# Performance work log

Measured on AMD Instinct MI355X. Metric: run time of the kernel, lower is better.

## Reference

```python
import jax, jax.numpy as jnp
import numpy as np

B, S, H, O, K = 32, 2048, 768, 768, 64


def setup_inputs() -> dict:
    key = jax.random.key(0)
    k0, k1, k2, k3, k4 = jax.random.split(key, 5)
    hidden = jax.random.normal(k0, (B, S, H), dtype=jnp.float32)
    token_idxs = jnp.sort(jax.random.randint(k1, (B, K), 0, S), axis=1)
    subject_hidden = jax.random.normal(k2, (B, H), dtype=jnp.float32)
    Wa = jax.random.normal(k3, (2 * H, 1), dtype=jnp.float32) * 0.02
    ba = jnp.zeros((1,), dtype=jnp.float32)
    Wo = jax.random.normal(k4, (H, O), dtype=jnp.float32) * 0.02
    bo = jnp.zeros((O,), dtype=jnp.float32)
    return {"hidden": hidden, "token_idxs": token_idxs, "subject_hidden": subject_hidden,
            "Wa": Wa, "ba": ba, "Wo": Wo, "bo": bo}


def reference(hidden, token_idxs, subject_hidden, Wa, ba, Wo, bo):
    b, s, h = hidden.shape
    # binary token mask [B,S] from per-example index lists (duplicates collapse to 1)
    mask = jnp.zeros((b, s), hidden.dtype).at[jnp.arange(b)[:, None], token_idxs].set(1.0)
    m3 = mask[:, :, None]                                  # [B,S,1]
    masked = hidden * m3                                   # masked_hidden
    subj_rep = subject_hidden[:, None, :] * m3             # broadcast + mask, no repeat
    # alignment_model(concat(subj, masked)) done as split matmul to avoid [B,S,2H]
    scores = subj_rep @ Wa[:h] + masked @ Wa[h:] + ba      # [B,S,1]
    # masked softmax over the selected tokens only (dim=0 over selected entries == seq axis)
    logits = jnp.where(m3 > 0, scores, jnp.float32(-1e9))
    attention_weights = jax.nn.softmax(logits, axis=1) * m3  # exact zeros off-mask
    pooled = jnp.einsum("bsh,bs->bh", masked, attention_weights[:, :, 0])
    transformed = jnp.tanh(pooled @ Wo + bo)
    return transformed, attention_weights
```

## Files before the change

kernel.cpp:

```cpp
#include <hip/hip_runtime.h>
#include <cmath>

#define Bb 32
#define Ss 2048
#define Hh 768
#define Oo 768
#define Kk 64

__global__ __launch_bounds__(256) void attn_pool_kernel(
    const float* __restrict__ hidden,
    const int*   __restrict__ idxs,
    const float* __restrict__ subj,
    const float* __restrict__ Wa,
    const float* __restrict__ ba,
    float* __restrict__ aw_out,
    float* __restrict__ pooled)
{
    const int b    = blockIdx.x;
    const int tid  = threadIdx.x;
    const int lane = tid & 63;
    const int wave = tid >> 6;

    __shared__ int   s_idx[Kk];
    __shared__ float s_aw[Kk];
    __shared__ float s_red[4];
    __shared__ float s_const;

    float4* awz = (float4*)(aw_out + (size_t)b * Ss);
    for (int i = tid; i < Ss / 4; i += 256) awz[i] = make_float4(0.f, 0.f, 0.f, 0.f);

    if (tid < Kk) s_idx[tid] = idxs[b * Kk + tid];
    __syncthreads();

    {
        float p = 0.f;
        for (int h = tid; h < Hh; h += 256)
            p += subj[b * Hh + h] * Wa[h];
        #pragma unroll
        for (int m = 32; m >= 1; m >>= 1) p += __shfl_xor(p, m);
        if (lane == 0) s_red[wave] = p;
        __syncthreads();
        if (tid == 0) s_const = s_red[0] + s_red[1] + s_red[2] + s_red[3] + ba[0];
        __syncthreads();
    }

    for (int j = wave; j < Kk; j += 4) {
        const float* row = hidden + ((size_t)b * Ss + s_idx[j]) * Hh;
        float p = 0.f;
        #pragma unroll
        for (int t = 0; t < Hh / 64; ++t)
            p += row[lane + 64 * t] * Wa[Hh + lane + 64 * t];
        #pragma unroll
        for (int m = 32; m >= 1; m >>= 1) p += __shfl_xor(p, m);
        if (lane == 0) s_aw[j] = p + s_const;
    }
    __syncthreads();

    if (wave == 0) {
        const int j = lane;
        const bool active = (j == 0) || (s_idx[j] != s_idx[j - 1]);
        float sc = active ? s_aw[j] : -3.0e38f;
        float mx = sc;
        #pragma unroll
        for (int m = 32; m >= 1; m >>= 1) mx = fmaxf(mx, __shfl_xor(mx, m));
        float e = active ? expf(sc - mx) : 0.f;
        float sum = e;
        #pragma unroll
        for (int m = 32; m >= 1; m >>= 1) sum += __shfl_xor(sum, m);
        const float aw = e / sum;
        s_aw[j] = aw;
        if (active) aw_out[(size_t)b * Ss + s_idx[j]] = aw;
    }
    __syncthreads();

    for (int h = tid; h < Hh; h += 256) {
        float acc = 0.f;
        #pragma unroll 8
        for (int j = 0; j < Kk; ++j)
            acc += s_aw[j] * hidden[((size_t)b * Ss + s_idx[j]) * Hh + h];
        pooled[b * Hh + h] = acc;
    }
}

__global__ __launch_bounds__(64) void gemm_tanh_kernel(
    const float* __restrict__ pooled,
    const float* __restrict__ Wo,
    const float* __restrict__ bo,
    float* __restrict__ out)
{
    const int b     = blockIdx.x / (Oo / 64);
    const int chunk = blockIdx.x % (Oo / 64);
    const int o     = chunk * 64 + threadIdx.x;

    __shared__ float p[Hh];
    float4* p4 = (float4*)p;
    const float4* src = (const float4*)(pooled + b * Hh);
    for (int i = threadIdx.x; i < Hh / 4; i += 64) p4[i] = src[i];
    __syncthreads();

    float a0 = 0.f, a1 = 0.f, a2 = 0.f, a3 = 0.f;
    #pragma unroll 4
    for (int h = 0; h < Hh; h += 4) {
        const float4 pv = *(const float4*)&p[h];
        a0 = fmaf(pv.x, Wo[(h + 0) * Oo + o], a0);
        a1 = fmaf(pv.y, Wo[(h + 1) * Oo + o], a1);
        a2 = fmaf(pv.z, Wo[(h + 2) * Oo + o], a2);
        a3 = fmaf(pv.w, Wo[(h + 3) * Oo + o], a3);
    }
    out[b * Oo + o] = tanhf(a0 + a1 + a2 + a3 + bo[o]);
}

extern "C" void kernel_launch(void* const* d_in, const int* in_sizes, int n_in,
                              void* d_out, int out_size, void* d_ws, size_t ws_size,
                              hipStream_t stream) {
    const float* hidden = (const float*)d_in[0];
    const int*   idxs   = (const int*)d_in[1];
    const float* subj   = (const float*)d_in[2];
    const float* Wa     = (const float*)d_in[3];
    const float* ba     = (const float*)d_in[4];
    const float* Wo     = (const float*)d_in[5];
    const float* bo     = (const float*)d_in[6];

    float* out    = (float*)d_out;
    float* aw_out = out + Bb * Oo;
    float* pooled = (float*)d_ws;

    attn_pool_kernel<<<Bb, 256, 0, stream>>>(hidden, idxs, subj, Wa, ba, aw_out, pooled);
    gemm_tanh_kernel<<<Bb * (Oo / 64), 64, 0, stream>>>(pooled, Wo, bo, out);
}
```

Measured before the change: 286.2 us.

## Split attention pooling into scores, softmax and fused pool-GEMM kernels for parallelism

The single 32-block attention kernel is replaced by a 512-block score kernel, with one wave per selected token and float4 loads, plus a small softmax kernel. A pooling+output GEMM kernel follows, where each of 96 blocks recomputes the pooled vector for its batch row and covers a 256-wide output slice. The aim is to spread the gather and score work across many more CUs than the 32 batch blocks could use. In exchange it adds a kernel launch, and the pooled gather is repeated three times per batch.

```diff
diff --git a/kernel.cpp b/kernel.cpp
--- a/kernel.cpp
+++ b/kernel.cpp
@@ -7,107 +7,131 @@
 #define Oo 768
 #define Kk 64
 
-__global__ __launch_bounds__(256) void attn_pool_kernel(
+__global__ __launch_bounds__(256) void scores_kernel(
     const float* __restrict__ hidden,
+    const int*   __restrict__ idxs,
+    const float* __restrict__ Wa,
+    float* __restrict__ scores,
+    float* __restrict__ aw_out)
+{
+    const int tid  = threadIdx.x;
+    const int lane = tid & 63;
+    const int wid  = blockIdx.x * 4 + (tid >> 6);
+    const int gid  = blockIdx.x * 256 + tid;
+
+    if (gid < (Bb * Ss / 4))
+        ((float4*)aw_out)[gid] = make_float4(0.f, 0.f, 0.f, 0.f);
+
+    const int b = wid >> 6;
+    const int j = wid & 63;
+    const int t_idx = idxs[b * Kk + j];
+
+    const float4* row4 = (const float4*)(hidden + ((size_t)b * Ss + t_idx) * Hh);
+    const float4* wa4  = (const float4*)(Wa + Hh);
+    float p = 0.f;
+    #pragma unroll
+    for (int t = 0; t < 3; ++t) {
+        const float4 r = row4[lane + 64 * t];
+        const float4 w = wa4[lane + 64 * t];
+        p += r.x * w.x + r.y * w.y + r.z * w.z + r.w * w.w;
+    }
+    #pragma unroll
+    for (int m = 32; m >= 1; m >>= 1) p += __shfl_xor(p, m);
+    if (lane == 0) scores[wid] = p;
+}
+
+__global__ __launch_bounds__(64) void softmax_kernel(
     const int*   __restrict__ idxs,
     const float* __restrict__ subj,
     const float* __restrict__ Wa,
     const float* __restrict__ ba,
-    float* __restrict__ aw_out,
-    float* __restrict__ pooled)
+    const float* __restrict__ scores,
+    float* __restrict__ aw,
+    float* __restrict__ aw_out)
 {
-    const int b    = blockIdx.x;
-    const int tid  = threadIdx.x;
-    const int lane = tid & 63;
-    const int wave = tid >> 6;
+    const int b = blockIdx.x;
+    const int j = threadIdx.x;
 
-    __shared__ int   s_idx[Kk];
-    __shared__ float s_aw[Kk];
-    __shared__ float s_red[4];
-    __shared__ float s_const;
+    const float4* s4  = (const float4*)(subj + b * Hh);
+    const float4* wa4 = (const float4*)Wa;
+    float p = 0.f;
+    #pragma unroll
+    for (int t = 0; t < 3; ++t) {
+        const float4 r = s4[j + 64 * t];
+        const float4 w = wa4[j + 64 * t];
+        p += r.x * w.x + r.y * w.y + r.z * w.z + r.w * w.w;
+    }
+    #pragma unroll
+    for (int m = 32; m >= 1; m >>= 1) p += __shfl_xor(p, m);
+    const float sconst = p + ba[0];
 
-    float4* awz = (float4*)(aw_out + (size_t)b * Ss);
-    for (int i = tid; i < Ss / 4; i += 256) awz[i] = make_float4(0.f, 0.f, 0.f, 0.f);
+    const int  myidx   = idxs[b * Kk + j];
+    const int  previdx = (j > 0) ? idxs[b * Kk + j - 1] : -1;
+    const bool active  = (j == 0) || (myidx != previdx);
 
-    if (tid < Kk) s_idx[tid] = idxs[b * Kk + tid];
-    __syncthreads();
+    float sc = active ? (scores[b * Kk + j] + sconst) : -3.0e38f;
+    float mx = sc;
+    #pragma unroll
+    for (int m = 32; m >= 1; m >>= 1) mx = fmaxf(mx, __shfl_xor(mx, m));
+    const float e = active ? expf(sc - mx) : 0.f;
+    float sum = e;
+    #pragma unroll
+    for (int m = 32; m >= 1; m >>= 1) sum += __shfl_xor(sum, m);
+    const float w = e / sum;
 
-    {
-        float p = 0.f;
-        for (int h = tid; h < Hh; h += 256)
-            p += subj[b * Hh + h] * Wa[h];
-        #pragma unroll
-        for (int m = 32; m >= 1; m >>= 1) p += __shfl_xor(p, m);
-        if (lane == 0) s_red[wave] = p;
-        __syncthreads();
-        if (tid == 0) s_const = s_red[0] + s_red[1] + s_red[2] + s_red[3] + ba[0];
-        __syncthreads();
-    }
-
-    for (int j = wave; j < Kk; j += 4) {
-        const float* row = hidden + ((size_t)b * Ss + s_idx[j]) * Hh;
-        float p = 0.f;
-        #pragma unroll
-        for (int t = 0; t < Hh / 64; ++t)
-            p += row[lane + 64 * t] * Wa[Hh + lane + 64 * t];
-        #pragma unroll
-        for (int m = 32; m >= 1; m >>= 1) p += __shfl_xor(p, m);
-        if (lane == 0) s_aw[j] = p + s_const;
-    }
-    __syncthreads();
-
-    if (wave == 0) {
-        const int j = lane;
-        const bool active = (j == 0) || (s_idx[j] != s_idx[j - 1]);
-        float sc = active ? s_aw[j] : -3.0e38f;
-        float mx = sc;
-        #pragma unroll
-        for (int m = 32; m >= 1; m >>= 1) mx = fmaxf(mx, __shfl_xor(mx, m));
-        float e = active ? expf(sc - mx) : 0.f;
-        float sum = e;
-        #pragma unroll
-        for (int m = 32; m >= 1; m >>= 1) sum += __shfl_xor(sum, m);
-        const float aw = e / sum;
-        s_aw[j] = aw;
-        if (active) aw_out[(size_t)b * Ss + s_idx[j]] = aw;
-    }
-    __syncthreads();
-
-    for (int h = tid; h < Hh; h += 256) {
-        float acc = 0.f;
-        #pragma unroll 8
-        for (int j = 0; j < Kk; ++j)
-            acc += s_aw[j] * hidden[((size_t)b * Ss + s_idx[j]) * Hh + h];
-        pooled[b * Hh + h] = acc;
-    }
+    aw[b * Kk + j] = w;
+    if (active) aw_out[(size_t)b * Ss + myidx] = w;
 }
 
-__global__ __launch_bounds__(64) void gemm_tanh_kernel(
-    const float* __restrict__ pooled,
+__global__ __launch_bounds__(1024) void pool_gemm_kernel(
+    const float* __restrict__ hidden,
+    const int*   __restrict__ idxs,
+    const float* __restrict__ aw,
     const float* __restrict__ Wo,
     const float* __restrict__ bo,
     float* __restrict__ out)
 {
-    const int b     = blockIdx.x / (Oo / 64);
-    const int chunk = blockIdx.x % (Oo / 64);
-    const int o     = chunk * 64 + threadIdx.x;
+    const int b   = blockIdx.x / 3;
+    const int oc  = blockIdx.x % 3;
+    const int tid = threadIdx.x;
 
-    __shared__ float p[Hh];
-    float4* p4 = (float4*)p;
-    const float4* src = (const float4*)(pooled + b * Hh);
-    for (int i = threadIdx.x; i < Hh / 4; i += 64) p4[i] = src[i];
+    __shared__ float s_aw[Kk];
+    __shared__ int   s_idx[Kk];
+    __shared__ float s_pool[Hh];
+    __shared__ float s_part[4 * 256];
+
+    if (tid < Kk) {
+        s_aw[tid]  = aw[b * Kk + tid];
+        s_idx[tid] = idxs[b * Kk + tid];
+    }
     __syncthreads();
 
-    float a0 = 0.f, a1 = 0.f, a2 = 0.f, a3 = 0.f;
-    #pragma unroll 4
-    for (int h = 0; h < Hh; h += 4) {
-        const float4 pv = *(const float4*)&p[h];
-        a0 = fmaf(pv.x, Wo[(h + 0) * Oo + o], a0);
-        a1 = fmaf(pv.y, Wo[(h + 1) * Oo + o], a1);
-        a2 = fmaf(pv.z, Wo[(h + 2) * Oo + o], a2);
-        a3 = fmaf(pv.w, Wo[(h + 3) * Oo + o], a3);
+    if (tid < Hh) {
+        float acc = 0.f;
+        #pragma unroll 8
+        for (int j = 0; j < Kk; ++j)
+            acc += s_aw[j] * hidden[((size_t)b * Ss + s_idx[j]) * Hh + tid];
+        s_pool[tid] = acc;
     }
-    out[b * Oo + o] = tanhf(a0 + a1 + a2 + a3 + bo[o]);
+    __syncthreads();
+
+    const int ol = tid & 255;
+    const int o  = oc * 256 + ol;
+    const int hg = tid >> 8;
+    const int h0 = hg * 192;
+    float acc = 0.f;
+    #pragma unroll 8
+    for (int h = h0; h < h0 + 192; ++h)
+        acc = fmaf(s_pool[h], Wo[h * Oo + o], acc);
+    s_part[hg * 256 + ol] = acc;
+    __syncthreads();
+
+    if (tid < 256) {
+        const int oo = oc * 256 + tid;
+        const float s = s_part[tid] + s_part[256 + tid] + s_part[512 + tid]
+                      + s_part[768 + tid] + bo[oo];
+        out[b * Oo + oo] = tanhf(s);
+    }
 }
 
 extern "C" void kernel_launch(void* const* d_in, const int* in_sizes, int n_in,
@@ -123,8 +147,10 @@
 
     float* out    = (float*)d_out;
     float* aw_out = out + Bb * Oo;
-    float* pooled = (float*)d_ws;
+    float* scores = (float*)d_ws;
+    float* aw     = scores + Bb * Kk;
 
-    attn_pool_kernel<<<Bb, 256, 0, stream>>>(hidden, idxs, subj, Wa, ba, aw_out, pooled);
-    gemm_tanh_kernel<<<Bb * (Oo / 64), 64, 0, stream>>>(pooled, Wo, bo, out);
+    scores_kernel <<<512, 256, 0, stream>>>(hidden, idxs, Wa, scores, aw_out);
+    softmax_kernel<<<Bb, 64, 0, stream>>>(idxs, subj, Wa, ba, scores, aw, aw_out);
+    pool_gemm_kernel<<<Bb * 3, 1024, 0, stream>>>(hidden, idxs, aw, Wo, bo, out);
 }
```

Result: faster. 262.6 us (-8.3%).
